# Performance work log

Hardware: AMD Instinct MI355X
Metric: run time of the kernel (lower is better)

## Reference

```python
import jax, jax.numpy as jnp
import numpy as np

SEQ, B, XD, HD, ZD = 256, 128, 128, 1024, 64


def setup_inputs() -> dict:
    key = jax.random.key(0)
    ks = jax.random.split(key, 32)
    w = lambda k, shape: (jax.random.normal(k, shape, jnp.float32) * 0.02)
    inp = {
        "x": jax.random.uniform(ks[0], (SEQ, B, XD), jnp.float32),
        "eps": jax.random.normal(ks[1], (SEQ, B, ZD), jnp.float32),
        "phi_x_W": w(ks[2], (HD, XD)),   "phi_x_b": jnp.zeros((HD,), jnp.float32),
        "enc_W": w(ks[3], (HD, 2 * HD)), "enc_b": jnp.zeros((HD,), jnp.float32),
        "enc_mean_W": w(ks[4], (ZD, HD)), "enc_mean_b": jnp.zeros((ZD,), jnp.float32),
        "enc_std_W": w(ks[5], (ZD, HD)),  "enc_std_b": jnp.zeros((ZD,), jnp.float32),
        "prior_W": w(ks[6], (HD, HD)),   "prior_b": jnp.zeros((HD,), jnp.float32),
        "prior_mean_W": w(ks[7], (ZD, HD)), "prior_mean_b": jnp.zeros((ZD,), jnp.float32),
        "prior_std_W": w(ks[8], (ZD, HD)),  "prior_std_b": jnp.zeros((ZD,), jnp.float32),
        "phi_z_W": w(ks[9], (HD, ZD)),   "phi_z_b": jnp.zeros((HD,), jnp.float32),
        "dec1_W": w(ks[10], (HD, 2 * HD)), "dec1_b": jnp.zeros((HD,), jnp.float32),
        "dec2_W": w(ks[11], (XD, HD)),     "dec2_b": jnp.zeros((XD,), jnp.float32),
        "gru_Wi": w(ks[12], (3 * HD, 2 * HD)), "gru_Wh": w(ks[13], (3 * HD, HD)),
        "gru_bi": jnp.zeros((3 * HD,), jnp.float32), "gru_bh": jnp.zeros((3 * HD,), jnp.float32),
    }
    return inp


def _lin(x, W, b):
    return x @ W.T + b


def _vrnn(x, eps, phi_x_W, phi_x_b, enc_W, enc_b, enc_mean_W, enc_mean_b,
          enc_std_W, enc_std_b, prior_W, prior_b, prior_mean_W, prior_mean_b,
          prior_std_W, prior_std_b, phi_z_W, phi_z_b, dec1_W, dec1_b,
          dec2_W, dec2_b, gru_Wi, gru_Wh, gru_bi, gru_bh):
    batch = x.shape[1]
    h0 = jnp.zeros((batch, gru_Wh.shape[1]), x.dtype)

    def step(h, inp):
        x_t, eps_t = inp
        phi_x_t = jax.nn.relu(_lin(x_t, phi_x_W, phi_x_b))
        prior_t = jax.nn.relu(_lin(h, prior_W, prior_b))
        prior_mean_t = _lin(prior_t, prior_mean_W, prior_mean_b)
        prior_std_t = jnp.exp(0.5 * _lin(prior_t, prior_std_W, prior_std_b))
        enc_t = jax.nn.relu(_lin(jnp.concatenate([phi_x_t, h], axis=1), enc_W, enc_b))
        enc_mean_t = _lin(enc_t, enc_mean_W, enc_mean_b)
        enc_std_t = jnp.exp(0.5 * _lin(enc_t, enc_std_W, enc_std_b))
        z_t = enc_mean_t + eps_t * enc_std_t
        phi_z_t = jax.nn.relu(_lin(z_t, phi_z_W, phi_z_b))
        dec_h = jax.nn.relu(_lin(jnp.concatenate([phi_z_t, h], axis=1), dec1_W, dec1_b))
        logits_t = _lin(dec_h, dec2_W, dec2_b)  # sigmoid(logits) is the reconstruction
        # GRU cell (PyTorch gate ordering r, z, n)
        u_t = jnp.concatenate([phi_x_t, phi_z_t], axis=1)
        gi = _lin(u_t, gru_Wi, gru_bi)
        gh = _lin(h, gru_Wh, gru_bh)
        hd = h.shape[1]
        i_r, i_z, i_n = gi[:, :hd], gi[:, hd:2 * hd], gi[:, 2 * hd:]
        h_r, h_z, h_n = gh[:, :hd], gh[:, hd:2 * hd], gh[:, 2 * hd:]
        r = jax.nn.sigmoid(i_r + h_r)
        zg = jax.nn.sigmoid(i_z + h_z)
        n = jnp.tanh(i_n + r * h_n)
        h_new = (1.0 - zg) * n + zg * h
        # per-step losses (sum reduction, as in the torch code)
        # BCE(sigmoid(l), x) = x*softplus(-l) + (1-x)*softplus(l)
        recon_t = jnp.sum(x_t * jax.nn.softplus(-logits_t) + (1.0 - x_t) * jax.nn.softplus(logits_t))
        kld_t = -0.5 * jnp.sum(1.0 + 2.0 * jnp.log(enc_std_t)
                               - (enc_mean_t - prior_mean_t) ** 2
                               - (enc_std_t / prior_std_t) ** 2)
        return h_new, (logits_t, recon_t, kld_t)

    _, (logits, recon_ts, kld_ts) = jax.lax.scan(step, h0, (x, eps))
    recon_loss = jnp.sum(recon_ts) / batch
    kld_loss = jnp.sum(kld_ts) / batch
    x_recon = jax.nn.sigmoid(logits)
    return recon_loss, kld_loss, x_recon


def reference(x, eps, phi_x_W, phi_x_b, enc_W, enc_b, enc_mean_W, enc_mean_b,
              enc_std_W, enc_std_b, prior_W, prior_b, prior_mean_W, prior_mean_b,
              prior_std_W, prior_std_b, phi_z_W, phi_z_b, dec1_W, dec1_b,
              dec2_W, dec2_b, gru_Wi, gru_Wh, gru_bi, gru_bh):
    return _vrnn(x, eps, phi_x_W, phi_x_b, enc_W, enc_b, enc_mean_W, enc_mean_b,
                 enc_std_W, enc_std_b, prior_W, prior_b, prior_mean_W, prior_mean_b,
                 prior_std_W, prior_std_b, phi_z_W, phi_z_b, dec1_W, dec1_b,
                 dec2_W, dec2_b, gru_Wi, gru_Wh, gru_bi, gru_bh)
```

## Files before the change

kernel.cpp:

```cpp
#include <hip/hip_runtime.h>
#include <algorithm>

typedef __bf16 bf16;
typedef __bf16 bf16x8 __attribute__((ext_vector_type(8)));
typedef float f32x4 __attribute__((ext_vector_type(4)));
typedef unsigned long long u64;

#define SEQ 256
#define BATCH 128
#define XD 128
#define HD 1024
#define ZD 64
#define MROWS (SEQ * BATCH)
#define BH (BATCH * HD)
#define B3 (BATCH * 3072)
#define DYN_LDS 154432
#define NBLK 256

__device__ __forceinline__ f32x4 mfma16(bf16x8 a, bf16x8 b, f32x4 c) {
  return __builtin_amdgcn_mfma_f32_16x16x32_bf16(a, b, c, 0, 0, 0);
}
__device__ __forceinline__ float sigmoidf_(float x) { return 1.f / (1.f + __expf(-x)); }

__device__ __forceinline__ void cst16(bf16* p, bf16x8 v) {
  asm volatile("global_store_dwordx4 %0, %1, off sc0 sc1" ::"v"(p), "v"(v) : "memory");
}
__device__ __forceinline__ void cst16f(float* p, f32x4 v) {
  asm volatile("global_store_dwordx4 %0, %1, off sc0 sc1" ::"v"(p), "v"(v) : "memory");
}

__device__ __forceinline__ void gbar(unsigned* arr, unsigned* sum, unsigned serial) {
  asm volatile("s_waitcnt vmcnt(0) lgkmcnt(0)" ::: "memory");
  __syncthreads();
  const int tid = threadIdx.x;
  const int bid = blockIdx.x;
  if (tid == 0)
    __hip_atomic_store(arr + (size_t)bid * 32, serial, __ATOMIC_RELAXED,
                       __HIP_MEMORY_SCOPE_AGENT);
  if ((bid & 15) == 0 && tid < 16) {
    const unsigned* f = arr + (size_t)((bid & ~15) + tid) * 32;
    while (__hip_atomic_load(f, __ATOMIC_RELAXED, __HIP_MEMORY_SCOPE_AGENT) < serial)
      __builtin_amdgcn_s_sleep(2);
  }
  __syncthreads();
  if ((bid & 15) == 0 && tid == 0)
    __hip_atomic_store(sum + (size_t)(bid >> 4) * 32, serial, __ATOMIC_RELAXED,
                       __HIP_MEMORY_SCOPE_AGENT);
  if (tid < 16) {
    const unsigned* f = sum + (size_t)tid * 32;
    while (__hip_atomic_load(f, __ATOMIC_RELAXED, __HIP_MEMORY_SCOPE_AGENT) < serial)
      __builtin_amdgcn_s_sleep(2);
  }
  __builtin_amdgcn_fence(__ATOMIC_ACQUIRE, "agent");
  __syncthreads();
}

template <int MT, int NT>
__device__ __forceinline__ void mma_block(const bf16* __restrict__ a0, size_t aStride,
                                          const bf16* __restrict__ b0, size_t bStride,
                                          int K, f32x4 acc[MT][NT]) {
#pragma unroll 2
  for (int k = 0; k < K; k += 32) {
    bf16x8 af[MT], bfr[NT];
#pragma unroll
    for (int i = 0; i < MT; ++i) af[i] = *(const bf16x8*)(a0 + (size_t)i * aStride + k);
#pragma unroll
    for (int j = 0; j < NT; ++j) bfr[j] = *(const bf16x8*)(b0 + (size_t)j * bStride + k);
#pragma unroll
    for (int i = 0; i < MT; ++i)
#pragma unroll
      for (int j = 0; j < NT; ++j) acc[i][j] = mfma16(af[i], bfr[j], acc[i][j]);
  }
}

__global__ void cvt_k(bf16* __restrict__ dst, const float* __restrict__ src, long n,
                      int cols, int src_ld, int col_off) {
  long i = (long)blockIdx.x * blockDim.x + threadIdx.x;
  long stride = (long)gridDim.x * blockDim.x;
  for (; i < n; i += stride) {
    long row = i / cols;
    int c = (int)(i - row * cols);
    dst[i] = (bf16)src[row * (long)src_ld + col_off + c];
  }
}

struct Epi {
  bf16* C;
  float* Cf;
  const float* bias;
  const bf16* add;
  int relu;
  int ldc;
};

template <int MT, int NT>
__global__ void gemm_bt(const bf16* __restrict__ A, int lda, const bf16* __restrict__ B,
                        int ldb, int M, int N, int K, Epi e) {
  const int lane = threadIdx.x & 63;
  const int r = lane & 15, kb = lane >> 4;
  const int gw = blockIdx.x * (blockDim.x >> 6) + (threadIdx.x >> 6);
  const int nw = gridDim.x * (blockDim.x >> 6);
  const int ntm = M / (16 * MT), ntn = N / (16 * NT);
  for (int task = gw; task < ntm * ntn; task += nw) {
    int mt = task % ntm, nt = task / ntm;
    int m0 = mt * 16 * MT, n0 = nt * 16 * NT;
    f32x4 acc[MT][NT] = {};
    const bf16* a0 = A + (size_t)(m0 + r) * lda + kb * 8;
    const bf16* b0 = B + (size_t)(n0 + r) * ldb + kb * 8;
    mma_block<MT, NT>(a0, (size_t)16 * lda, b0, (size_t)16 * ldb, K, acc);
#pragma unroll
    for (int i = 0; i < MT; ++i)
#pragma unroll
      for (int j = 0; j < NT; ++j)
#pragma unroll
        for (int q = 0; q < 4; ++q) {
          size_t gm = (size_t)m0 + i * 16 + kb * 4 + q;
          int gn = n0 + j * 16 + r;
          float v = acc[i][j][q] + e.bias[gn];
          if (e.add) v += (float)e.add[gm * e.ldc + gn];
          if (e.relu) v = fmaxf(v, 0.f);
          if (e.Cf) e.Cf[gm * e.ldc + gn] = v;
          else e.C[gm * e.ldc + gn] = (bf16)v;
        }
  }
}

struct LoopP {
  const bf16 *WA, *WB, *WPZ, *WIZ, *WIX, *WXX, *WPX, *WDZ, *WD2, *XBF;
  bf16 *HB, *PT, *ET, *PHIX, *ENCX, *PHIZ, *DHP, *DECH;
  float *H, *GH, *GIX, *KLD, *RPART, *out;
  unsigned *ARR, *SUM, *PFLAG;
  const float *eps, *x;
  const float *prior_b, *gru_bh, *gru_bi, *pm_b, *ps_b, *em_b, *es_b, *pz_b, *phx_b,
      *enc_b, *dec1_b, *dec2_b;
};

__device__ __forceinline__ void stage1024(char* lds, int off, const bf16* src) {
  for (int c = threadIdx.x; c < 2048; c += 512) {
    int kg = c & 127, rr = c >> 7;
    *(float4*)(lds + off + (((kg << 4) + rr) << 4)) =
        *(const float4*)(src + (size_t)rr * 1024 + kg * 8);
  }
}

template <int KK>
__device__ __forceinline__ void load_af(bf16x8* af, const bf16* A, int row, int lda, int k0,
                                        int kb) {
#pragma unroll
  for (int kk = 0; kk < KK; ++kk)
    af[kk] = *(const bf16x8*)(A + (size_t)row * lda + k0 + kk * 32 + kb * 8);
}

template <int NU>
__device__ __forceinline__ void run_units(const bf16* Arow, const char* slab0, f32x4* acc,
                                          int r, int kb) {
  bf16x8 af[32];
#pragma unroll
  for (int kk = 0; kk < 32; ++kk) af[kk] = *(const bf16x8*)(Arow + kk * 32 + kb * 8);
#pragma unroll
  for (int u = 0; u < NU; ++u)
#pragma unroll
    for (int kk = 0; kk < 32; ++kk)
      acc[u] = mfma16(af[kk],
                      *(const bf16x8*)(slab0 + u * 32768 + ((((kk * 4 + kb) << 4) + r) << 4)),
                      acc[u]);
}

__device__ __forceinline__ void xpose2(float* wscr, const f32x4* acc, int ua, int r, int kb,
                                       int urow, int cb, int usel, float* vals) {
#pragma unroll
  for (int tdx = 0; tdx < 2; ++tdx) {
    f32x4 a = acc[ua + tdx];
    int base = tdx * 328 + (kb * 4) * 20 + r;
#pragma unroll
    for (int q = 0; q < 4; ++q) wscr[base + q * 20] = a[q];
  }
  asm volatile("s_waitcnt lgkmcnt(0)" ::: "memory");
  __builtin_amdgcn_sched_barrier(0);
  int rb = usel * 328 + urow * 20 + cb;
#pragma unroll
  for (int j = 0; j < 8; ++j) vals[j] = wscr[rb + j];
}

__global__ void __launch_bounds__(512, 1) vrnn_loop(LoopP p) {
  extern __shared__ char lds[];
  const int tid = threadIdx.x, lane = tid & 63, wv = tid >> 6;
  const int r = lane & 15, kb = lane >> 4;
  const int urow = (lane & 31) >> 1, cb = (lane & 1) * 8, usel = lane >> 5;
  const int b = blockIdx.x;
  unsigned bs = 0;

  int cls, uid0 = 0, gizj = 0, wpxb = 0;
  if (b < 8) cls = 0;
  else if (b < 104) { cls = 1; uid0 = 4 * (b - 8); }
  else if (b < 120) { cls = 2; uid0 = 4 * (b - 104); }
  else if (b < 122) { cls = 3; wpxb = b - 120; }
  else if (b < 186) { cls = 4; uid0 = 4 * (b - 122); }
  else if (b < 188) { cls = 5; uid0 = 4 * (b - 186); }
  else if (b < 252) { cls = 6; gizj = b - 188; }
  else cls = 7;

  float* wscr = (float*)(lds + 131072) + wv * 656;

  if (cls == 0) {
    for (int c = tid; c < 8192; c += 512) {
      int kg = c & 7, rr = (c >> 3) & 15, u = c >> 7;
      *(float4*)(lds + u * 2048 + (((kg << 4) + rr) << 4)) =
          *(const float4*)(p.WPZ + (size_t)(u * 16 + rr) * 64 + kg * 8);
    }
  } else if (cls == 1) {
    for (int u = 0; u < 4; ++u) stage1024(lds, u * 32768, p.WA + (size_t)(uid0 + u) * 16 * 1024);
  } else if (cls == 2) {
    for (int u = 0; u < 4; ++u) stage1024(lds, u * 32768, p.WDZ + (size_t)(uid0 + u) * 16 * 1024);
  } else if (cls == 3) {
    for (int c = tid; c < 8192; c += 512) {
      int u = c >> 8, kg = c & 15, rr = (c >> 4) & 15;
      *(float4*)(lds + u * 4096 + (((kg << 4) + rr) << 4)) =
          *(const float4*)(p.WPX + (size_t)((wpxb * 32 + u) * 16 + rr) * 128 + kg * 8);
    }
  } else if (cls == 4) {
    for (int u = 0; u < 4; ++u) {
      int uid = uid0 + u;
      const bf16* src = (uid < 64) ? p.WXX + (size_t)uid * 16 * 1024
                                   : p.WIX + (size_t)(uid - 64) * 16 * 1024;
      stage1024(lds, u * 32768, src);
    }
  } else if (cls == 5) {
    for (int u = 0; u < 4; ++u) stage1024(lds, u * 32768, p.WD2 + (size_t)(uid0 + u) * 16 * 1024);
  } else if (cls == 6) {
    for (int g = 0; g < 3; ++g)
      stage1024(lds, g * 32768, p.WIZ + (size_t)(g * 1024 + gizj * 16) * 1024);
  }
  __syncthreads();

  for (int t = 0; t < SEQ; ++t) {
    const int cur = t & 1, oth = cur ^ 1;

    if (cls == 1) {
      const bf16* Arow = p.HB + (size_t)(wv * 16 + r) * HD;
      f32x4 acc[4] = {};
      run_units<4>(Arow, lds, acc, r, kb);
#pragma unroll
      for (int up = 0; up < 4; up += 2) {
        float vals[8];
        xpose2(wscr, acc, up, r, kb, urow, cb, usel, vals);
        int uid = uid0 + up + usel;
        int gm = wv * 16 + urow;
        if (uid < 64) {
          int gn = uid * 16 + cb;
          bf16x8 o;
#pragma unroll
          for (int j = 0; j < 8; ++j) o[j] = (bf16)fmaxf(vals[j] + p.prior_b[gn + j], 0.f);
          cst16(&p.PT[gm * HD + gn], o);
        } else if (uid < 128) {
          int c = (uid - 64) * 16 + cb;
          bf16x8 ex = *(const bf16x8*)(p.ENCX + (size_t)cur * BH + gm * HD + c);
          bf16x8 o;
#pragma unroll
          for (int j = 0; j < 8; ++j) o[j] = (bf16)fmaxf(vals[j] + (float)ex[j], 0.f);
          cst16(&p.ET[gm * HD + c], o);
        } else if (uid < 320) {
          int c = (uid - 128) * 16 + cb;
          f32x4 g0, g1;
#pragma unroll
          for (int j = 0; j < 4; ++j) g0[j] = vals[j] + p.gru_bh[c + j];
#pragma unroll
          for (int j = 0; j < 4; ++j) g1[j] = vals[4 + j] + p.gru_bh[c + 4 + j];
          cst16f(&p.GH[gm * 3072 + c], g0);
          cst16f(&p.GH[gm * 3072 + c + 4], g1);
        } else {
          int c = (uid - 320) * 16 + cb;
          bf16x8 o;
#pragma unroll
          for (int j = 0; j < 8; ++j) o[j] = (bf16)vals[j];
          cst16(&p.DHP[(size_t)cur * BH + gm * HD + c], o);
        }
      }
    } else if (cls == 2 && t > 0) {
      const bf16* Arow = p.PHIZ + (size_t)oth * BH + (size_t)(wv * 16 + r) * HD;
      f32x4 acc[4] = {};
      run_units<4>(Arow, lds, acc, r, kb);
#pragma unroll
      for (int up = 0; up < 4; up += 2) {
        float vals[8];
        xpose2(wscr, acc, up, r, kb, urow, cb, usel, vals);
        int c = (uid0 + up + usel) * 16 + cb;
        int gm = wv * 16 + urow;
        bf16x8 dh = *(const bf16x8*)(p.DHP + (size_t)oth * BH + gm * HD + c);
        bf16x8 o;
#pragma unroll
        for (int j = 0; j < 8; ++j)
          o[j] = (bf16)fmaxf(vals[j] + (float)dh[j] + p.dec1_b[c + j], 0.f);
        cst16(&p.DECH[gm * HD + c], o);
      }
    } else if (cls == 3 && t < SEQ - 1) {
      bf16x8 af2[4];
      load_af<4>(af2, p.XBF + (size_t)(t + 1) * BATCH * XD, wv * 16 + r, 128, 0, kb);
#pragma unroll 1
      for (int up = 0; up < 32; up += 2) {
        f32x4 acc2[2] = {};
#pragma unroll
        for (int tdx = 0; tdx < 2; ++tdx)
#pragma unroll
          for (int kk = 0; kk < 4; ++kk)
            acc2[tdx] = mfma16(af2[kk],
                               *(const bf16x8*)(lds + (up + tdx) * 4096 +
                                                ((((kk * 4 + kb) << 4) + r) << 4)),
                               acc2[tdx]);
        float vals[8];
        xpose2(wscr, acc2, 0, r, kb, urow, cb, usel, vals);
        int gn = (wpxb * 32 + up + usel) * 16 + cb;
        int gm = wv * 16 + urow;
        bf16x8 o;
#pragma unroll
        for (int j = 0; j < 8; ++j) o[j] = (bf16)fmaxf(vals[j] + p.phx_b[gn + j], 0.f);
        cst16(&p.PHIX[gm * HD + gn], o);
      }
    }
    gbar(p.ARR, p.SUM, ++bs);

    if (cls == 0) {
      const int m0 = b * 16;
      const int mat = wv & 3, half = wv >> 2;
      float* sm = (float*)(lds + 131072);
      bf16* zs = (bf16*)(lds + 152064);
      float* red = (float*)(lds + 154368);
      {
        const bf16* Arow = ((mat < 2) ? p.PT : p.ET) + (size_t)(m0 + r) * HD;
        bf16x8 af[32];
#pragma unroll
        for (int kk = 0; kk < 32; ++kk) af[kk] = *(const bf16x8*)(Arow + kk * 32 + kb * 8);
        const float* bw = mat == 0 ? p.pm_b : mat == 1 ? p.ps_b : mat == 2 ? p.em_b : p.es_b;
#pragma unroll 1
        for (int nt = 0; nt < 2; ++nt) {
          int colb = half * 32 + nt * 16;
          f32x4 acc = {};
#pragma unroll
          for (int kk = 0; kk < 32; ++kk)
            acc = mfma16(af[kk],
                         *(const bf16x8*)(p.WB + (size_t)(mat * 64 + colb + r) * 1024 +
                                          kk * 32 + kb * 8),
                         acc);
#pragma unroll
          for (int qq = 0; qq < 4; ++qq)
            sm[mat * 1024 + (kb * 4 + qq) * 64 + colb + r] = acc[qq] + bw[colb + r];
        }
      }
      __syncthreads();
      float kacc = 0.f;
      for (int e = tid; e < 1024; e += 512) {
        int row = e >> 6, col = e & 63;
        float pm = sm[row * 64 + col], ps = sm[1024 + row * 64 + col];
        float em = sm[2048 + row * 64 + col], es = sm[3072 + row * 64 + col];
        float ev = p.eps[((size_t)t * BATCH + m0 + row) * ZD + col];
        zs[row * 72 + col] = (bf16)(em + ev * __expf(0.5f * es));
        float dm = em - pm;
        kacc += 1.f + es - dm * dm - __expf(es - ps);
      }
#pragma unroll
      for (int off = 32; off; off >>= 1) kacc += __shfl_down(kacc, off, 64);
      if (lane == 0) red[wv] = kacc;
      __syncthreads();
      if (tid == 0) {
        float ss = 0.f;
        for (int i = 0; i < 8; ++i) ss += red[i];
        p.KLD[t * 8 + b] = ss;
      }
      bf16x8 afz[2];
      afz[0] = *(const bf16x8*)(zs + r * 72 + kb * 8);
      afz[1] = *(const bf16x8*)(zs + r * 72 + 32 + kb * 8);
#pragma unroll 1
      for (int jp = 0; jp < 8; jp += 2) {
        f32x4 acc2[2] = {};
#pragma unroll
        for (int tdx = 0; tdx < 2; ++tdx) {
          int u = wv * 8 + jp + tdx;
#pragma unroll
          for (int kk = 0; kk < 2; ++kk)
            acc2[tdx] = mfma16(afz[kk],
                               *(const bf16x8*)(lds + u * 2048 +
                                                ((((kk * 4 + kb) << 4) + r) << 4)),
                               acc2[tdx]);
        }
        float vals[8];
        xpose2(wscr, acc2, 0, r, kb, urow, cb, usel, vals);
        int gn = (wv * 8 + jp + usel) * 16 + cb;
        int gm = m0 + urow;
        bf16x8 o;
#pragma unroll
        for (int j = 0; j < 8; ++j) o[j] = (bf16)fmaxf(vals[j] + p.pz_b[gn + j], 0.f);
        cst16(&p.PHIZ[(size_t)cur * BH + gm * HD + gn], o);
      }
      asm volatile("s_waitcnt vmcnt(0)" ::: "memory");
      __syncthreads();
      if (tid == 0)
        __hip_atomic_store(p.PFLAG + (size_t)b * 32, (unsigned)(t + 1), __ATOMIC_RELAXED,
                           __HIP_MEMORY_SCOPE_AGENT);
    } else if (cls == 4 && t < SEQ - 1) {
      const bf16* Arow = p.PHIX + (size_t)(wv * 16 + r) * HD;
      f32x4 acc[4] = {};
      run_units<4>(Arow, lds, acc, r, kb);
#pragma unroll
      for (int up = 0; up < 4; up += 2) {
        float vals[8];
        xpose2(wscr, acc, up, r, kb, urow, cb, usel, vals);
        int uid = uid0 + up + usel;
        int gm = wv * 16 + urow;
        if (uid < 64) {
          int c = uid * 16 + cb;
          bf16x8 o;
#pragma unroll
          for (int j = 0; j < 8; ++j) o[j] = (bf16)(vals[j] + p.enc_b[c + j]);
          cst16(&p.ENCX[(size_t)oth * BH + gm * HD + c], o);
        } else {
          int c = (uid - 64) * 16 + cb;
          f32x4 g0, g1;
#pragma unroll
          for (int j = 0; j < 4; ++j) g0[j] = vals[j] + p.gru_bi[c + j];
#pragma unroll
          for (int j = 0; j < 4; ++j) g1[j] = vals[4 + j] + p.gru_bi[c + 4 + j];
          cst16f(&p.GIX[(size_t)oth * B3 + gm * 3072 + c], g0);
          cst16f(&p.GIX[(size_t)oth * B3 + gm * 3072 + c + 4], g1);
        }
      }
    } else if (cls == 5 && t > 0) {
      const bf16* Arow = p.DECH + (size_t)(wv * 16 + r) * HD;
      f32x4 acc[4] = {};
      run_units<4>(Arow, lds, acc, r, kb);
      float racc = 0.f;
#pragma unroll
      for (int up = 0; up < 4; up += 2) {
        float vals[8];
        xpose2(wscr, acc, up, r, kb, urow, cb, usel, vals);
        int c = (uid0 + up + usel) * 16 + cb;
        int gm = wv * 16 + urow;
        size_t oi = ((size_t)(t - 1) * BATCH + gm) * XD + c;
#pragma unroll
        for (int j = 0; j < 8; ++j) {
          float l = vals[j] + p.dec2_b[c + j];
          p.out[2 + oi + j] = sigmoidf_(l);
          float spp = fmaxf(l, 0.f) + log1pf(__expf(-fabsf(l)));
          racc += spp - p.x[oi + j] * l;
        }
      }
#pragma unroll
      for (int off = 32; off; off >>= 1) racc += __shfl_down(racc, off, 64);
      if (lane == 0) p.RPART[(t - 1) * 64 + uid0 * 2 + wv] = racc;
    } else if (cls == 6) {
      if (tid < 8) {
        const unsigned* f = p.PFLAG + (size_t)tid * 32;
        while (__hip_atomic_load(f, __ATOMIC_RELAXED, __HIP_MEMORY_SCOPE_AGENT) <
               (unsigned)(t + 1))
          __builtin_amdgcn_s_sleep(1);
      }
      __syncthreads();
      __builtin_amdgcn_sched_barrier(0);
      float* scR = (float*)(lds + 98304);
      const int khalf = wv >> 2, mtg = wv & 3;
#pragma unroll 1
      for (int pass = 0; pass < 2; ++pass) {
        int mt = mtg + 4 * pass;
        const bf16* Arow = p.PHIZ + (size_t)cur * BH + (size_t)(mt * 16 + r) * HD;
        bf16x8 af[16];
#pragma unroll
        for (int kk = 0; kk < 16; ++kk)
          af[kk] = *(const bf16x8*)(Arow + khalf * 512 + kk * 32 + kb * 8);
        f32x4 a3[3] = {};
#pragma unroll
        for (int kk = 0; kk < 16; ++kk) {
          bf16x8 a = af[kk];
#pragma unroll
          for (int g = 0; g < 3; ++g)
            a3[g] = mfma16(a,
                           *(const bf16x8*)(lds + g * 32768 +
                                            (((((khalf * 16 + kk) * 4 + kb) << 4) + r) << 4)),
                           a3[g]);
        }
#pragma unroll
        for (int g = 0; g < 3; ++g)
#pragma unroll
          for (int q = 0; q < 4; ++q)
            scR[khalf * 3072 + mtg * 768 + g * 256 + (kb * 4 + q) * 16 + r] = a3[g][q];
        __syncthreads();
        if (tid < 128) {
          int mtg2 = tid >> 5, row = (tid & 31) >> 1, cb2 = (tid & 1) * 8;
          int gm = (mtg2 + 4 * pass) * 16 + row;
          int c = gizj * 16 + cb2;
          int base = mtg2 * 768 + row * 16 + cb2;
          float iv[3][8], hv[3][8];
#pragma unroll
          for (int g = 0; g < 3; ++g) {
            f32x4 i0 = *(const f32x4*)(p.GIX + (size_t)cur * B3 + gm * 3072 + g * 1024 + c);
            f32x4 i1 = *(const f32x4*)(p.GIX + (size_t)cur * B3 + gm * 3072 + g * 1024 + c + 4);
            f32x4 h0 = *(const f32x4*)(p.GH + gm * 3072 + g * 1024 + c);
            f32x4 h1 = *(const f32x4*)(p.GH + gm * 3072 + g * 1024 + c + 4);
#pragma unroll
            for (int j = 0; j < 8; ++j) {
              float part = scR[base + g * 256 + j] + scR[3072 + base + g * 256 + j];
              iv[g][j] = part + ((j < 4) ? i0[j] : i1[j - 4]);
              hv[g][j] = (j < 4) ? h0[j] : h1[j - 4];
            }
          }
          f32x4 hc0 = *(const f32x4*)(p.H + gm * HD + c);
          f32x4 hc1 = *(const f32x4*)(p.H + gm * HD + c + 4);
          f32x4 hn0, hn1;
          bf16x8 o;
#pragma unroll
          for (int j = 0; j < 8; ++j) {
            float rr2 = sigmoidf_(iv[0][j] + hv[0][j]);
            float zg = sigmoidf_(iv[1][j] + hv[1][j]);
            float nn = tanhf(iv[2][j] + rr2 * hv[2][j]);
            float hvv = (j < 4) ? hc0[j] : hc1[j - 4];
            float hnew = (1.f - zg) * nn + zg * hvv;
            if (j < 4) hn0[j] = hnew; else hn1[j - 4] = hnew;
            o[j] = (bf16)hnew;
          }
          *(f32x4*)(p.H + gm * HD + c) = hn0;
          *(f32x4*)(p.H + gm * HD + c + 4) = hn1;
          cst16(&p.HB[gm * HD + c], o);
        }
        __syncthreads();
      }
    }
    gbar(p.ARR, p.SUM, ++bs);
  }
}

__global__ void dec2_last(const bf16* __restrict__ A, const bf16* __restrict__ W,
                          const float* __restrict__ x, const float* __restrict__ b2,
                          float* __restrict__ out, float* __restrict__ rpart) {
  const int lane = threadIdx.x & 63;
  const int r = lane & 15, kb = lane >> 4;
  const int w = blockIdx.x * 4 + (threadIdx.x >> 6);
  const int m0 = (w & 7) * 16, n0 = (w >> 3) * 16;
  f32x4 acc[1][1] = {};
  const bf16* a0 = A + (size_t)(m0 + r) * HD + kb * 8;
  const bf16* b0 = W + (size_t)(n0 + r) * HD + kb * 8;
  mma_block<1, 1>(a0, 0, b0, (size_t)16 * HD, HD, acc);
  float racc = 0.f;
#pragma unroll
  for (int q = 0; q < 4; ++q) {
    int gm = m0 + kb * 4 + q, gn = n0 + r;
    float l = acc[0][0][q] + b2[gn];
    size_t oi = ((size_t)255 * BATCH + gm) * XD + gn;
    out[2 + oi] = sigmoidf_(l);
    float spp = fmaxf(l, 0.f) + log1pf(__expf(-fabsf(l)));
    racc += spp - x[oi] * l;
  }
#pragma unroll
  for (int off = 32; off; off >>= 1) racc += __shfl_down(racc, off, 64);
  if (lane == 0) rpart[255 * 64 + w] = racc;
}

__global__ void finalize_k(const float* __restrict__ rp, const float* __restrict__ kp,
                           float* __restrict__ out) {
  __shared__ float s[256];
  int tid = threadIdx.x;
  float a = 0.f;
  for (int i = tid; i < 256 * 64; i += 256) a += rp[i];
  s[tid] = a;
  __syncthreads();
  for (int off = 128; off > 0; off >>= 1) {
    if (tid < off) s[tid] += s[tid + off];
    __syncthreads();
  }
  if (tid == 0) out[0] = s[0] / (float)BATCH;
  __syncthreads();
  float bb = 0.f;
  for (int i = tid; i < 2048; i += 256) bb += kp[i];
  s[tid] = bb;
  __syncthreads();
  for (int off = 128; off > 0; off >>= 1) {
    if (tid < off) s[tid] += s[tid + off];
    __syncthreads();
  }
  if (tid == 0) out[1] = -0.5f * s[0] / (float)BATCH;
}

__global__ void sentinel_k(float* out) {
  if (threadIdx.x == 0) { out[0] = 1e9f; out[1] = 1e9f; }
}

extern "C" void kernel_launch(void* const* d_in, const int* in_sizes, int n_in, void* d_out,
                              int out_size, void* d_ws, size_t ws_size, hipStream_t stream) {
  const float* x = (const float*)d_in[0];
  const float* eps = (const float*)d_in[1];
  const float* phi_x_W = (const float*)d_in[2];
  const float* phi_x_b = (const float*)d_in[3];
  const float* enc_W = (const float*)d_in[4];
  const float* enc_b = (const float*)d_in[5];
  const float* enc_mean_W = (const float*)d_in[6];
  const float* enc_mean_b = (const float*)d_in[7];
  const float* enc_std_W = (const float*)d_in[8];
  const float* enc_std_b = (const float*)d_in[9];
  const float* prior_W = (const float*)d_in[10];
  const float* prior_b = (const float*)d_in[11];
  const float* prior_mean_W = (const float*)d_in[12];
  const float* prior_mean_b = (const float*)d_in[13];
  const float* prior_std_W = (const float*)d_in[14];
  const float* prior_std_b = (const float*)d_in[15];
  const float* phi_z_W = (const float*)d_in[16];
  const float* phi_z_b = (const float*)d_in[17];
  const float* dec1_W = (const float*)d_in[18];
  const float* dec1_b = (const float*)d_in[19];
  const float* dec2_W = (const float*)d_in[20];
  const float* dec2_b = (const float*)d_in[21];
  const float* gru_Wi = (const float*)d_in[22];
  const float* gru_Wh = (const float*)d_in[23];
  const float* gru_bi = (const float*)d_in[24];
  const float* gru_bh = (const float*)d_in[25];
  float* out = (float*)d_out;

  char* w = (char*)d_ws;
  auto carve = [&](size_t bytes) {
    char* pp = w;
    w += (bytes + 255) & ~(size_t)255;
    return pp;
  };
  bf16* WA = (bf16*)carve((size_t)6144 * HD * 2);
  bf16* WB = (bf16*)carve((size_t)256 * HD * 2);
  bf16* WPZ = (bf16*)carve((size_t)HD * ZD * 2);
  bf16* WIZ = (bf16*)carve((size_t)3072 * HD * 2);
  bf16* WIX = (bf16*)carve((size_t)3072 * HD * 2);
  bf16* WXX = (bf16*)carve((size_t)HD * HD * 2);
  bf16* WPX = (bf16*)carve((size_t)HD * XD * 2);
  bf16* WDZ = (bf16*)carve((size_t)HD * HD * 2);
  bf16* WD2 = (bf16*)carve((size_t)XD * HD * 2);
  bf16* XBF = (bf16*)carve((size_t)MROWS * XD * 2);
  float* H = (float*)carve((size_t)BH * 4);
  bf16* HB = (bf16*)carve((size_t)BH * 2);
  bf16* PT = (bf16*)carve((size_t)BH * 2);
  bf16* ET = (bf16*)carve((size_t)BH * 2);
  float* GH = (float*)carve((size_t)B3 * 4);
  bf16* PHIX = (bf16*)carve((size_t)BH * 2);
  bf16* ENCX = (bf16*)carve((size_t)2 * BH * 2);
  bf16* PHIZ = (bf16*)carve((size_t)2 * BH * 2);
  bf16* DHP = (bf16*)carve((size_t)2 * BH * 2);
  bf16* DECH = (bf16*)carve((size_t)BH * 2);
  float* GIX = (float*)carve((size_t)2 * B3 * 4);
  float* KLD = (float*)carve((size_t)SEQ * 8 * 4);
  float* RPART = (float*)carve((size_t)SEQ * 64 * 4);
  unsigned* ARR = (unsigned*)carve((size_t)NBLK * 32 * 4);
  unsigned* SUM = (unsigned*)carve((size_t)16 * 32 * 4);
  unsigned* PFLAG = (unsigned*)carve((size_t)8 * 32 * 4);
  if ((size_t)(w - (char*)d_ws) > ws_size) {
    sentinel_k<<<1, 64, 0, stream>>>(out);
    return;
  }

  auto cvt = [&](bf16* dst, const float* src, long n, int cols, int ld, int off) {
    int grid = (int)std::min((n + 255) / 256, (long)2048);
    cvt_k<<<grid, 256, 0, stream>>>(dst, src, n, cols, ld, off);
  };
  cvt(WA, prior_W, (long)HD * HD, HD, HD, 0);
  cvt(WA + (size_t)HD * HD, enc_W, (long)HD * HD, HD, 2 * HD, HD);
  cvt(WA + (size_t)2048 * HD, gru_Wh, (long)3072 * HD, HD, HD, 0);
  cvt(WA + (size_t)5120 * HD, dec1_W, (long)HD * HD, HD, 2 * HD, HD);
  cvt(WB, prior_mean_W, (long)ZD * HD, HD, HD, 0);
  cvt(WB + (size_t)64 * HD, prior_std_W, (long)ZD * HD, HD, HD, 0);
  cvt(WB + (size_t)128 * HD, enc_mean_W, (long)ZD * HD, HD, HD, 0);
  cvt(WB + (size_t)192 * HD, enc_std_W, (long)ZD * HD, HD, HD, 0);
  cvt(WPZ, phi_z_W, (long)HD * ZD, ZD, ZD, 0);
  cvt(WIZ, gru_Wi, (long)3072 * HD, HD, 2 * HD, HD);
  cvt(WIX, gru_Wi, (long)3072 * HD, HD, 2 * HD, 0);
  cvt(WXX, enc_W, (long)HD * HD, HD, 2 * HD, 0);
  cvt(WPX, phi_x_W, (long)HD * XD, XD, XD, 0);
  cvt(WDZ, dec1_W, (long)HD * HD, HD, 2 * HD, 0);
  cvt(WD2, dec2_W, (long)XD * HD, HD, HD, 0);
  cvt(XBF, x, (long)MROWS * XD, XD, XD, 0);

  hipMemsetAsync(H, 0, (size_t)BH * 4, stream);
  hipMemsetAsync(HB, 0, (size_t)BH * 2, stream);
  hipMemsetAsync(RPART, 0, (size_t)SEQ * 64 * 4, stream);
  hipMemsetAsync(ARR, 0, (size_t)NBLK * 32 * 4, stream);
  hipMemsetAsync(SUM, 0, (size_t)16 * 32 * 4, stream);
  hipMemsetAsync(PFLAG, 0, (size_t)8 * 32 * 4, stream);

  Epi e1{PHIX, nullptr, phi_x_b, nullptr, 1, HD};
  gemm_bt<2, 2><<<32, 256, 0, stream>>>(XBF, XD, WPX, XD, BATCH, HD, XD, e1);
  Epi e2{ENCX, nullptr, enc_b, nullptr, 0, HD};
  gemm_bt<2, 2><<<32, 256, 0, stream>>>(PHIX, HD, WXX, HD, BATCH, HD, HD, e2);
  Epi e3{nullptr, GIX, gru_bi, nullptr, 0, 3072};
  gemm_bt<2, 2><<<96, 256, 0, stream>>>(PHIX, HD, WIX, HD, BATCH, 3072, HD, e3);

  LoopP lp;
  lp.WA = WA; lp.WB = WB; lp.WPZ = WPZ; lp.WIZ = WIZ; lp.WIX = WIX; lp.WXX = WXX;
  lp.WPX = WPX; lp.WDZ = WDZ; lp.WD2 = WD2; lp.XBF = XBF;
  lp.HB = HB; lp.PT = PT; lp.ET = ET; lp.PHIX = PHIX; lp.ENCX = ENCX; lp.PHIZ = PHIZ;
  lp.DHP = DHP; lp.DECH = DECH;
  lp.H = H; lp.GH = GH; lp.GIX = GIX; lp.KLD = KLD; lp.RPART = RPART; lp.out = out;
  lp.ARR = ARR; lp.SUM = SUM; lp.PFLAG = PFLAG;
  lp.eps = eps; lp.x = x;
  lp.prior_b = prior_b; lp.gru_bh = gru_bh; lp.gru_bi = gru_bi;
  lp.pm_b = prior_mean_b; lp.ps_b = prior_std_b; lp.em_b = enc_mean_b; lp.es_b = enc_std_b;
  lp.pz_b = phi_z_b; lp.phx_b = phi_x_b; lp.enc_b = enc_b; lp.dec1_b = dec1_b;
  lp.dec2_b = dec2_b;

  hipFuncSetAttribute(reinterpret_cast<const void*>(vrnn_loop),
                      hipFuncAttributeMaxDynamicSharedMemorySize, DYN_LDS);
  void* args[] = {&lp};
  hipLaunchCooperativeKernel(reinterpret_cast<const void*>(vrnn_loop), dim3(NBLK), dim3(512),
                             args, DYN_LDS, stream);

  Epi e4{DECH, nullptr, dec1_b, DHP + (size_t)1 * BH, 1, HD};
  gemm_bt<2, 2><<<32, 256, 0, stream>>>(PHIZ + (size_t)1 * BH, HD, WDZ, HD, BATCH, HD, HD, e4);
  dec2_last<<<16, 256, 0, stream>>>(DECH, WD2, x, dec2_b, out, RPART);
  finalize_k<<<1, 256, 0, stream>>>(RPART, KLD, out);
}
```

Before: 20.99 ms.

## Replace mid-step grid barrier with per-block producer flags and double-buffer HB

Removes the first of the two grid-wide barriers inside each timestep. Consumer block classes now spin on per-producer flags in a new FLG array, and producer classes publish a step counter after draining their stores. The bf16 hidden state HB becomes double-buffered so the GRU block can write the new state while prior/encoder blocks still read the previous one. This is meant to cut barrier latency and let independent stages overlap, at the cost of more flag traffic and fragile dependency indexing.

```diff
diff --git a/kernel.cpp b/kernel.cpp
--- a/kernel.cpp
+++ b/kernel.cpp
@@ -27,6 +27,11 @@
 }
 __device__ __forceinline__ void cst16f(float* p, f32x4 v) {
   asm volatile("global_store_dwordx4 %0, %1, off sc0 sc1" ::"v"(p), "v"(v) : "memory");
+}
+
+__device__ __forceinline__ void flagwait1(const unsigned* f, unsigned want) {
+  while (__hip_atomic_load(f, __ATOMIC_RELAXED, __HIP_MEMORY_SCOPE_AGENT) < want)
+    __builtin_amdgcn_s_sleep(1);
 }
 
 __device__ __forceinline__ void gbar(unsigned* arr, unsigned* sum, unsigned serial) {
@@ -129,7 +134,7 @@
   const bf16 *WA, *WB, *WPZ, *WIZ, *WIX, *WXX, *WPX, *WDZ, *WD2, *XBF;
   bf16 *HB, *PT, *ET, *PHIX, *ENCX, *PHIZ, *DHP, *DECH;
   float *H, *GH, *GIX, *KLD, *RPART, *out;
-  unsigned *ARR, *SUM, *PFLAG;
+  unsigned *ARR, *SUM, *FLG;
   const float *eps, *x;
   const float *prior_b, *gru_bh, *gru_bi, *pm_b, *ps_b, *em_b, *es_b, *pz_b, *phx_b,
       *enc_b, *dec1_b, *dec2_b;
@@ -237,7 +242,7 @@
     const int cur = t & 1, oth = cur ^ 1;
 
     if (cls == 1) {
-      const bf16* Arow = p.HB + (size_t)(wv * 16 + r) * HD;
+      const bf16* Arow = p.HB + (size_t)oth * BH + (size_t)(wv * 16 + r) * HD;
       f32x4 acc[4] = {};
       run_units<4>(Arow, lds, acc, r, kb);
 #pragma unroll
@@ -276,50 +281,70 @@
           cst16(&p.DHP[(size_t)cur * BH + gm * HD + c], o);
         }
       }
-    } else if (cls == 2 && t > 0) {
-      const bf16* Arow = p.PHIZ + (size_t)oth * BH + (size_t)(wv * 16 + r) * HD;
-      f32x4 acc[4] = {};
-      run_units<4>(Arow, lds, acc, r, kb);
-#pragma unroll
-      for (int up = 0; up < 4; up += 2) {
-        float vals[8];
-        xpose2(wscr, acc, up, r, kb, urow, cb, usel, vals);
-        int c = (uid0 + up + usel) * 16 + cb;
-        int gm = wv * 16 + urow;
-        bf16x8 dh = *(const bf16x8*)(p.DHP + (size_t)oth * BH + gm * HD + c);
-        bf16x8 o;
-#pragma unroll
-        for (int j = 0; j < 8; ++j)
-          o[j] = (bf16)fmaxf(vals[j] + (float)dh[j] + p.dec1_b[c + j], 0.f);
-        cst16(&p.DECH[gm * HD + c], o);
-      }
-    } else if (cls == 3 && t < SEQ - 1) {
-      bf16x8 af2[4];
-      load_af<4>(af2, p.XBF + (size_t)(t + 1) * BATCH * XD, wv * 16 + r, 128, 0, kb);
+      asm volatile("s_waitcnt vmcnt(0)" ::: "memory");
+      __syncthreads();
+      if (tid == 0)
+        __hip_atomic_store(p.FLG + (size_t)b * 32, (unsigned)(t + 1), __ATOMIC_RELAXED,
+                           __HIP_MEMORY_SCOPE_AGENT);
+    } else if (cls == 2) {
+      if (t > 0) {
+        const bf16* Arow = p.PHIZ + (size_t)oth * BH + (size_t)(wv * 16 + r) * HD;
+        f32x4 acc[4] = {};
+        run_units<4>(Arow, lds, acc, r, kb);
+#pragma unroll
+        for (int up = 0; up < 4; up += 2) {
+          float vals[8];
+          xpose2(wscr, acc, up, r, kb, urow, cb, usel, vals);
+          int c = (uid0 + up + usel) * 16 + cb;
+          int gm = wv * 16 + urow;
+          bf16x8 dh = *(const bf16x8*)(p.DHP + (size_t)oth * BH + gm * HD + c);
+          bf16x8 o;
+#pragma unroll
+          for (int j = 0; j < 8; ++j)
+            o[j] = (bf16)fmaxf(vals[j] + (float)dh[j] + p.dec1_b[c + j], 0.f);
+          cst16(&p.DECH[gm * HD + c], o);
+        }
+      }
+      asm volatile("s_waitcnt vmcnt(0)" ::: "memory");
+      __syncthreads();
+      if (tid == 0)
+        __hip_atomic_store(p.FLG + (size_t)b * 32, (unsigned)(t + 1), __ATOMIC_RELAXED,
+                           __HIP_MEMORY_SCOPE_AGENT);
+    } else if (cls == 3) {
+      if (t < SEQ - 1) {
+        bf16x8 af2[4];
+        load_af<4>(af2, p.XBF + (size_t)(t + 1) * BATCH * XD, wv * 16 + r, 128, 0, kb);
 #pragma unroll 1
-      for (int up = 0; up < 32; up += 2) {
-        f32x4 acc2[2] = {};
-#pragma unroll
-        for (int tdx = 0; tdx < 2; ++tdx)
-#pragma unroll
-          for (int kk = 0; kk < 4; ++kk)
-            acc2[tdx] = mfma16(af2[kk],
-                               *(const bf16x8*)(lds + (up + tdx) * 4096 +
-                                                ((((kk * 4 + kb) << 4) + r) << 4)),
-                               acc2[tdx]);
-        float vals[8];
-        xpose2(wscr, acc2, 0, r, kb, urow, cb, usel, vals);
-        int gn = (wpxb * 32 + up + usel) * 16 + cb;
-        int gm = wv * 16 + urow;
-        bf16x8 o;
-#pragma unroll
-        for (int j = 0; j < 8; ++j) o[j] = (bf16)fmaxf(vals[j] + p.phx_b[gn + j], 0.f);
-        cst16(&p.PHIX[gm * HD + gn], o);
-      }
-    }
-    gbar(p.ARR, p.SUM, ++bs);
-
-    if (cls == 0) {
+        for (int up = 0; up < 32; up += 2) {
+          f32x4 acc2[2] = {};
+#pragma unroll
+          for (int tdx = 0; tdx < 2; ++tdx)
+#pragma unroll
+            for (int kk = 0; kk < 4; ++kk)
+              acc2[tdx] = mfma16(af2[kk],
+                                 *(const bf16x8*)(lds + (up + tdx) * 4096 +
+                                                  ((((kk * 4 + kb) << 4) + r) << 4)),
+                                 acc2[tdx]);
+          float vals[8];
+          xpose2(wscr, acc2, 0, r, kb, urow, cb, usel, vals);
+          int gn = (wpxb * 32 + up + usel) * 16 + cb;
+          int gm = wv * 16 + urow;
+          bf16x8 o;
+#pragma unroll
+          for (int j = 0; j < 8; ++j) o[j] = (bf16)fmaxf(vals[j] + p.phx_b[gn + j], 0.f);
+          cst16(&p.PHIX[gm * HD + gn], o);
+        }
+      }
+      asm volatile("s_waitcnt vmcnt(0)" ::: "memory");
+      __syncthreads();
+      if (tid == 0)
+        __hip_atomic_store(p.FLG + (size_t)b * 32, (unsigned)(t + 1), __ATOMIC_RELAXED,
+                           __HIP_MEMORY_SCOPE_AGENT);
+    } else if (cls == 0) {
+      if (tid < 32) flagwait1(p.FLG + (size_t)(8 + tid) * 32, (unsigned)(t + 1));
+      __syncthreads();
+      __builtin_amdgcn_fence(__ATOMIC_ACQUIRE, "agent");
+      __builtin_amdgcn_sched_barrier(0);
       const int m0 = b * 16;
       const int mat = wv & 3, half = wv >> 2;
       float* sm = (float*)(lds + 131072);
@@ -394,66 +419,77 @@
       asm volatile("s_waitcnt vmcnt(0)" ::: "memory");
       __syncthreads();
       if (tid == 0)
-        __hip_atomic_store(p.PFLAG + (size_t)b * 32, (unsigned)(t + 1), __ATOMIC_RELAXED,
+        __hip_atomic_store(p.FLG + (size_t)b * 32, (unsigned)(t + 1), __ATOMIC_RELAXED,
                            __HIP_MEMORY_SCOPE_AGENT);
-    } else if (cls == 4 && t < SEQ - 1) {
-      const bf16* Arow = p.PHIX + (size_t)(wv * 16 + r) * HD;
-      f32x4 acc[4] = {};
-      run_units<4>(Arow, lds, acc, r, kb);
-#pragma unroll
-      for (int up = 0; up < 4; up += 2) {
-        float vals[8];
-        xpose2(wscr, acc, up, r, kb, urow, cb, usel, vals);
-        int uid = uid0 + up + usel;
-        int gm = wv * 16 + urow;
-        if (uid < 64) {
-          int c = uid * 16 + cb;
-          bf16x8 o;
-#pragma unroll
-          for (int j = 0; j < 8; ++j) o[j] = (bf16)(vals[j] + p.enc_b[c + j]);
-          cst16(&p.ENCX[(size_t)oth * BH + gm * HD + c], o);
-        } else {
-          int c = (uid - 64) * 16 + cb;
-          f32x4 g0, g1;
-#pragma unroll
-          for (int j = 0; j < 4; ++j) g0[j] = vals[j] + p.gru_bi[c + j];
-#pragma unroll
-          for (int j = 0; j < 4; ++j) g1[j] = vals[4 + j] + p.gru_bi[c + 4 + j];
-          cst16f(&p.GIX[(size_t)oth * B3 + gm * 3072 + c], g0);
-          cst16f(&p.GIX[(size_t)oth * B3 + gm * 3072 + c + 4], g1);
-        }
-      }
-    } else if (cls == 5 && t > 0) {
-      const bf16* Arow = p.DECH + (size_t)(wv * 16 + r) * HD;
-      f32x4 acc[4] = {};
-      run_units<4>(Arow, lds, acc, r, kb);
-      float racc = 0.f;
-#pragma unroll
-      for (int up = 0; up < 4; up += 2) {
-        float vals[8];
-        xpose2(wscr, acc, up, r, kb, urow, cb, usel, vals);
-        int c = (uid0 + up + usel) * 16 + cb;
-        int gm = wv * 16 + urow;
-        size_t oi = ((size_t)(t - 1) * BATCH + gm) * XD + c;
-#pragma unroll
-        for (int j = 0; j < 8; ++j) {
-          float l = vals[j] + p.dec2_b[c + j];
-          p.out[2 + oi + j] = sigmoidf_(l);
-          float spp = fmaxf(l, 0.f) + log1pf(__expf(-fabsf(l)));
-          racc += spp - p.x[oi + j] * l;
-        }
-      }
-#pragma unroll
-      for (int off = 32; off; off >>= 1) racc += __shfl_down(racc, off, 64);
-      if (lane == 0) p.RPART[(t - 1) * 64 + uid0 * 2 + wv] = racc;
+    } else if (cls == 4) {
+      if (tid < 2) flagwait1(p.FLG + (size_t)(120 + tid) * 32, (unsigned)(t + 1));
+      __syncthreads();
+      __builtin_amdgcn_fence(__ATOMIC_ACQUIRE, "agent");
+      __builtin_amdgcn_sched_barrier(0);
+      if (t < SEQ - 1) {
+        const bf16* Arow = p.PHIX + (size_t)(wv * 16 + r) * HD;
+        f32x4 acc[4] = {};
+        run_units<4>(Arow, lds, acc, r, kb);
+#pragma unroll
+        for (int up = 0; up < 4; up += 2) {
+          float vals[8];
+          xpose2(wscr, acc, up, r, kb, urow, cb, usel, vals);
+          int uid = uid0 + up + usel;
+          int gm = wv * 16 + urow;
+          if (uid < 64) {
+            int c = uid * 16 + cb;
+            bf16x8 o;
+#pragma unroll
+            for (int j = 0; j < 8; ++j) o[j] = (bf16)(vals[j] + p.enc_b[c + j]);
+            cst16(&p.ENCX[(size_t)oth * BH + gm * HD + c], o);
+          } else {
+            int c = (uid - 64) * 16 + cb;
+            f32x4 g0, g1;
+#pragma unroll
+            for (int j = 0; j < 4; ++j) g0[j] = vals[j] + p.gru_bi[c + j];
+#pragma unroll
+            for (int j = 0; j < 4; ++j) g1[j] = vals[4 + j] + p.gru_bi[c + 4 + j];
+            cst16f(&p.GIX[(size_t)oth * B3 + gm * 3072 + c], g0);
+            cst16f(&p.GIX[(size_t)oth * B3 + gm * 3072 + c + 4], g1);
+          }
+        }
+      }
+    } else if (cls == 5) {
+      if (tid < 16) flagwait1(p.FLG + (size_t)(104 + tid) * 32, (unsigned)(t + 1));
+      __syncthreads();
+      __builtin_amdgcn_fence(__ATOMIC_ACQUIRE, "agent");
+      __builtin_amdgcn_sched_barrier(0);
+      if (t > 0) {
+        const bf16* Arow = p.DECH + (size_t)(wv * 16 + r) * HD;
+        f32x4 acc[4] = {};
+        run_units<4>(Arow, lds, acc, r, kb);
+        float racc = 0.f;
+#pragma unroll
+        for (int up = 0; up < 4; up += 2) {
+          float vals[8];
+          xpose2(wscr, acc, up, r, kb, urow, cb, usel, vals);
+          int c = (uid0 + up + usel) * 16 + cb;
+          int gm = wv * 16 + urow;
+          size_t oi = ((size_t)(t - 1) * BATCH + gm) * XD + c;
+#pragma unroll
+          for (int j = 0; j < 8; ++j) {
+            float l = vals[j] + p.dec2_b[c + j];
+            p.out[2 + oi + j] = sigmoidf_(l);
+            float spp = fmaxf(l, 0.f) + log1pf(__expf(-fabsf(l)));
+            racc += spp - p.x[oi + j] * l;
+          }
+        }
+#pragma unroll
+        for (int off = 32; off; off >>= 1) racc += __shfl_down(racc, off, 64);
+        if (lane == 0) p.RPART[(t - 1) * 64 + uid0 * 2 + wv] = racc;
+      }
     } else if (cls == 6) {
-      if (tid < 8) {
-        const unsigned* f = p.PFLAG + (size_t)tid * 32;
-        while (__hip_atomic_load(f, __ATOMIC_RELAXED, __HIP_MEMORY_SCOPE_AGENT) <
-               (unsigned)(t + 1))
-          __builtin_amdgcn_s_sleep(1);
-      }
-      __syncthreads();
+      if (tid < 56) {
+        int idx = (tid < 48) ? (40 + tid) : (tid - 48);
+        flagwait1(p.FLG + (size_t)idx * 32, (unsigned)(t + 1));
+      }
+      __syncthreads();
+      __builtin_amdgcn_fence(__ATOMIC_ACQUIRE, "agent");
       __builtin_amdgcn_sched_barrier(0);
       float* scR = (float*)(lds + 98304);
       const int khalf = wv >> 2, mtg = wv & 3;
@@ -517,7 +553,7 @@
           }
           *(f32x4*)(p.H + gm * HD + c) = hn0;
           *(f32x4*)(p.H + gm * HD + c + 4) = hn1;
-          cst16(&p.HB[gm * HD + c], o);
+          cst16(&p.HB[(size_t)cur * BH + gm * HD + c], o);
         }
         __syncthreads();
       }
@@ -628,7 +664,7 @@
   bf16* WD2 = (bf16*)carve((size_t)XD * HD * 2);
   bf16* XBF = (bf16*)carve((size_t)MROWS * XD * 2);
   float* H = (float*)carve((size_t)BH * 4);
-  bf16* HB = (bf16*)carve((size_t)BH * 2);
+  bf16* HB = (bf16*)carve((size_t)2 * BH * 2);
   bf16* PT = (bf16*)carve((size_t)BH * 2);
   bf16* ET = (bf16*)carve((size_t)BH * 2);
   float* GH = (float*)carve((size_t)B3 * 4);
@@ -642,7 +678,7 @@
   float* RPART = (float*)carve((size_t)SEQ * 64 * 4);
   unsigned* ARR = (unsigned*)carve((size_t)NBLK * 32 * 4);
   unsigned* SUM = (unsigned*)carve((size_t)16 * 32 * 4);
-  unsigned* PFLAG = (unsigned*)carve((size_t)8 * 32 * 4);
+  unsigned* FLG = (unsigned*)carve((size_t)128 * 32 * 4);
   if ((size_t)(w - (char*)d_ws) > ws_size) {
     sentinel_k<<<1, 64, 0, stream>>>(out);
     return;
@@ -670,11 +706,11 @@
   cvt(XBF, x, (long)MROWS * XD, XD, XD, 0);
 
   hipMemsetAsync(H, 0, (size_t)BH * 4, stream);
-  hipMemsetAsync(HB, 0, (size_t)BH * 2, stream);
+  hipMemsetAsync(HB, 0, (size_t)2 * BH * 2, stream);
   hipMemsetAsync(RPART, 0, (size_t)SEQ * 64 * 4, stream);
   hipMemsetAsync(ARR, 0, (size_t)NBLK * 32 * 4, stream);
   hipMemsetAsync(SUM, 0, (size_t)16 * 32 * 4, stream);
-  hipMemsetAsync(PFLAG, 0, (size_t)8 * 32 * 4, stream);
+  hipMemsetAsync(FLG, 0, (size_t)128 * 32 * 4, stream);
 
   Epi e1{PHIX, nullptr, phi_x_b, nullptr, 1, HD};
   gemm_bt<2, 2><<<32, 256, 0, stream>>>(XBF, XD, WPX, XD, BATCH, HD, XD, e1);
@@ -689,7 +725,7 @@
   lp.HB = HB; lp.PT = PT; lp.ET = ET; lp.PHIX = PHIX; lp.ENCX = ENCX; lp.PHIZ = PHIZ;
   lp.DHP = DHP; lp.DECH = DECH;
   lp.H = H; lp.GH = GH; lp.GIX = GIX; lp.KLD = KLD; lp.RPART = RPART; lp.out = out;
-  lp.ARR = ARR; lp.SUM = SUM; lp.PFLAG = PFLAG;
+  lp.ARR = ARR; lp.SUM = SUM; lp.FLG = FLG;
   lp.eps = eps; lp.x = x;
   lp.prior_b = prior_b; lp.gru_bh = gru_bh; lp.gru_bi = gru_bi;
   lp.pm_b = prior_mean_b; lp.ps_b = prior_std_b; lp.em_b = enc_mean_b; lp.es_b = enc_std_b;
```

After: 18.36 ms. 1.14x faster.
